# Kernel tuning notes

Measured on AMD Instinct MI355X. Metric: run time of the kernel, lower is better.

The kernel has to match this reference:

```python
import jax, jax.numpy as jnp
import numpy as np

D_MODEL = 1024
N_HEADS = 16
HEAD_DIM = D_MODEL // N_HEADS


def setup_inputs() -> dict:
    key = jax.random.key(0)
    k_x, k_q, k_k, k_v = jax.random.split(key, 4)
    B, S = 2, 2048
    x = jax.random.normal(k_x, (B, S, D_MODEL), dtype=jnp.float32)
    # nn.Linear weights stored as [out, in]; we apply x @ W.T
    scale = 1.0 / np.sqrt(D_MODEL)
    W_q = jax.random.uniform(k_q, (D_MODEL, D_MODEL), jnp.float32, -scale, scale)
    W_k = jax.random.uniform(k_k, (D_MODEL, D_MODEL), jnp.float32, -scale, scale)
    W_v = jax.random.uniform(k_v, (D_MODEL, D_MODEL), jnp.float32, -scale, scale)
    return {"x": x, "W_q": W_q, "W_k": W_k, "W_v": W_v}


def reference(x, W_q, W_k, W_v):
    B, S, D = x.shape
    H, Hd = N_HEADS, HEAD_DIM
    # QKV projections (Linear with no bias): x @ W.T
    Q = (x @ W_q.T).reshape(B, S, H, Hd).transpose(0, 2, 1, 3)  # [B,H,S,Hd]
    K = (x @ W_k.T).reshape(B, S, H, Hd).transpose(0, 2, 1, 3)
    V = (x @ W_v.T).reshape(B, S, H, Hd).transpose(0, 2, 1, 3)
    scores = jnp.einsum("bhqd,bhkd->bhqk", Q, K) / jnp.sqrt(jnp.float32(Hd))
    attn = jax.nn.softmax(scores, axis=-1)
    out = jnp.einsum("bhqk,bhkd->bhqd", attn, V)  # [B,H,S,Hd]
    return out.transpose(0, 2, 1, 3).reshape(B, S, H * Hd)
```

## Files before the change

kernel.cpp:

```cpp
#include <hip/hip_runtime.h>
#include <stdint.h>


typedef __bf16 bf16x8 __attribute__((ext_vector_type(8)));
typedef __bf16 bf16x4 __attribute__((ext_vector_type(4)));
typedef float  f32x4  __attribute__((ext_vector_type(4)));

#define D_MODEL 1024
#define SEQ     2048
#define NHEAD   16
#define HDIM    64
#define BS      4096

__device__ __forceinline__ void load_lds16(const void* g, void* lds) {
  __builtin_amdgcn_global_load_lds(
      (__attribute__((address_space(1))) void*)(uintptr_t)g,
      (__attribute__((address_space(3))) void*)(uintptr_t)lds,
      16, 0, 0);
}

__global__ void cvt_f32_bf16(const float* __restrict__ in,
                             __bf16* __restrict__ out, int n4) {
  int i = blockIdx.x * blockDim.x + threadIdx.x;
  if (i < n4) {
    float4 v = ((const float4*)in)[i];
    bf16x4 o;
    o[0] = (__bf16)v.x; o[1] = (__bf16)v.y;
    o[2] = (__bf16)v.z; o[3] = (__bf16)v.w;
    ((bf16x4*)out)[i] = o;
  }
}

__global__ __launch_bounds__(256) void qkv_gemm(
    const __bf16* __restrict__ X,
    const __bf16* __restrict__ Wq, const __bf16* __restrict__ Wk,
    const __bf16* __restrict__ Wv,
    __bf16* __restrict__ Qb, __bf16* __restrict__ Kb, __bf16* __restrict__ Vt) {
  __shared__ __bf16 As[128 * 32];
  __shared__ __bf16 Bs[128 * 32];

  const __bf16* W = (blockIdx.z == 0) ? Wq : (blockIdx.z == 1) ? Wk : Wv;

  const int t    = threadIdx.x;
  const int wv   = t >> 6;
  const int lane = t & 63;
  const int l15  = lane & 15;
  const int quad = lane >> 4;
  const int m0   = blockIdx.y * 128;
  const int n0   = blockIdx.x * 128;
  const int wm   = (wv >> 1) * 64;
  const int wn   = (wv & 1) * 64;

  f32x4 acc[4][4] = {};

  for (int it = 0; it < 32; ++it) {
    const int k0 = it * 32;
#pragma unroll
    for (int p = 0; p < 2; ++p) {
      const int c   = p * 256 + t;
      const int row = c >> 2;
      const int ko  = (c & 3) * 8;
      const unsigned lb = (unsigned)((p * 256 + wv * 64) * 16);
      load_lds16(X + (size_t)(m0 + row) * D_MODEL + k0 + ko, (char*)As + lb);
      load_lds16(W + (size_t)(n0 + row) * D_MODEL + k0 + ko, (char*)Bs + lb);
    }
    __syncthreads();

    bf16x8 af[4], bfb[4];
#pragma unroll
    for (int i = 0; i < 4; ++i)
      af[i] = *(const bf16x8*)&As[(wm + i * 16 + l15) * 32 + quad * 8];
#pragma unroll
    for (int j = 0; j < 4; ++j)
      bfb[j] = *(const bf16x8*)&Bs[(wn + j * 16 + l15) * 32 + quad * 8];
#pragma unroll
    for (int i = 0; i < 4; ++i)
#pragma unroll
      for (int j = 0; j < 4; ++j)
        acc[i][j] = __builtin_amdgcn_mfma_f32_16x16x32_bf16(af[i], bfb[j],
                                                            acc[i][j], 0, 0, 0);
    __syncthreads();
  }

  if (blockIdx.z != 2) {
    __bf16* Out = (blockIdx.z == 0) ? Qb : Kb;
#pragma unroll
    for (int i = 0; i < 4; ++i) {
      const int rg = m0 + wm + i * 16 + quad * 4;
#pragma unroll
      for (int j = 0; j < 4; ++j) {
        const int cg = n0 + wn + j * 16 + l15;
#pragma unroll
        for (int r = 0; r < 4; ++r)
          Out[(size_t)(rg + r) * D_MODEL + cg] = (__bf16)acc[i][j][r];
      }
    }
  } else {
#pragma unroll
    for (int i = 0; i < 4; ++i) {
      const int mg = m0 + wm + i * 16 + quad * 4;
#pragma unroll
      for (int j = 0; j < 4; ++j) {
        const int ng = n0 + wn + j * 16 + l15;
        bf16x4 v;
#pragma unroll
        for (int r = 0; r < 4; ++r) v[r] = (__bf16)acc[i][j][r];
        *(bf16x4*)&Vt[(size_t)ng * BS + mg] = v;
      }
    }
  }
}

__global__ __launch_bounds__(256) void attn(
    const __bf16* __restrict__ Qb, const __bf16* __restrict__ Kb,
    const __bf16* __restrict__ Vt, float* __restrict__ out) {
  __shared__ __bf16 Ks[64 * 64];
  __shared__ __bf16 Vs[64 * 64];
  __shared__ __bf16 Ps[4][16][72];

  const int t    = threadIdx.x;
  const int wv   = t >> 6;
  const int lane = t & 63;
  const int l15  = lane & 15;
  const int quad = lane >> 4;
  const int h    = blockIdx.y;
  const size_t bo = (size_t)blockIdx.z * SEQ;
  const int q0   = blockIdx.x * 64 + wv * 16;
  const int hd0  = h * HDIM;

  bf16x8 qf[2];
#pragma unroll
  for (int c = 0; c < 2; ++c) {
    qf[c] = *(const bf16x8*)&Qb[(bo + q0 + l15) * D_MODEL + hd0 + c * 32 + quad * 8];
#pragma unroll
    for (int j = 0; j < 8; ++j)
      qf[c][j] = (__bf16)(0.125f * (float)qf[c][j]);
  }

  float lsum[4] = {0.f, 0.f, 0.f, 0.f};
  f32x4 o_acc[4] = {};

  const int swz = quad ^ (l15 & 7);
  const int swz4 = (quad + 4) ^ (l15 & 7);

  for (int kt = 0; kt < SEQ / 64; ++kt) {
    const int n0 = kt * 64;
#pragma unroll
    for (int p = 0; p < 2; ++p) {
      const int c   = p * 256 + t;
      const int row = c >> 3;
      const int cc  = (c & 7) ^ (row & 7);
      const unsigned lb = (unsigned)((p * 256 + wv * 64) * 16);
      load_lds16(Kb + (bo + n0 + row) * D_MODEL + hd0 + cc * 8, (char*)Ks + lb);
      load_lds16(Vt + (size_t)(hd0 + row) * BS + bo + n0 + cc * 8, (char*)Vs + lb);
    }
    __syncthreads();

    f32x4 s[4] = {};
#pragma unroll
    for (int nt = 0; nt < 4; ++nt) {
      const int r = nt * 16 + l15;
      bf16x8 kf0 = *(const bf16x8*)&Ks[(r * 8 + swz) * 8];
      bf16x8 kf1 = *(const bf16x8*)&Ks[(r * 8 + swz4) * 8];
      s[nt] = __builtin_amdgcn_mfma_f32_16x16x32_bf16(qf[0], kf0, s[nt], 0, 0, 0);
      s[nt] = __builtin_amdgcn_mfma_f32_16x16x32_bf16(qf[1], kf1, s[nt], 0, 0, 0);
    }

#pragma unroll
    for (int nt = 0; nt < 4; ++nt)
#pragma unroll
      for (int r = 0; r < 4; ++r) {
        float p = __expf(s[nt][r]);
        lsum[r] += p;
        Ps[wv][quad * 4 + r][nt * 16 + l15] = (__bf16)p;
      }

    bf16x8 pf0 = *(const bf16x8*)&Ps[wv][l15][quad * 8];
    bf16x8 pf1 = *(const bf16x8*)&Ps[wv][l15][32 + quad * 8];

#pragma unroll
    for (int tt = 0; tt < 4; ++tt) {
      const int r = tt * 16 + l15;
      bf16x8 vf0 = *(const bf16x8*)&Vs[(r * 8 + swz) * 8];
      bf16x8 vf1 = *(const bf16x8*)&Vs[(r * 8 + swz4) * 8];
      o_acc[tt] = __builtin_amdgcn_mfma_f32_16x16x32_bf16(pf0, vf0, o_acc[tt], 0, 0, 0);
      o_acc[tt] = __builtin_amdgcn_mfma_f32_16x16x32_bf16(pf1, vf1, o_acc[tt], 0, 0, 0);
    }
    __syncthreads();
  }

#pragma unroll
  for (int r = 0; r < 4; ++r) {
    float s = lsum[r];
    s += __shfl_xor(s, 1);
    s += __shfl_xor(s, 2);
    s += __shfl_xor(s, 4);
    s += __shfl_xor(s, 8);
    lsum[r] = s;
  }

#pragma unroll
  for (int r = 0; r < 4; ++r) {
    float inv = 1.f / lsum[r];
    const size_t row = bo + q0 + quad * 4 + r;
#pragma unroll
    for (int tt = 0; tt < 4; ++tt)
      out[row * D_MODEL + hd0 + tt * 16 + l15] = o_acc[tt][r] * inv;
  }
}

extern "C" void kernel_launch(void* const* d_in, const int* in_sizes, int n_in,
                              void* d_out, int out_size, void* d_ws, size_t ws_size,
                              hipStream_t stream) {
  const float* x  = (const float*)d_in[0];
  const float* Wq = (const float*)d_in[1];
  const float* Wk = (const float*)d_in[2];
  const float* Wv = (const float*)d_in[3];
  float* out = (float*)d_out;

  char* ws = (char*)d_ws;
  __bf16* xb  = (__bf16*)(ws);
  __bf16* wqb = (__bf16*)(ws + (8u  << 20));
  __bf16* wkb = (__bf16*)(ws + (10u << 20));
  __bf16* wvb = (__bf16*)(ws + (12u << 20));
  __bf16* Qbf = (__bf16*)(ws + (14u << 20));
  __bf16* Kbf = (__bf16*)(ws + (22u << 20));
  __bf16* Vt  = (__bf16*)(ws + (30u << 20));

  cvt_f32_bf16<<<4096, 256, 0, stream>>>(x,  xb,  4194304 / 4);
  cvt_f32_bf16<<<1024, 256, 0, stream>>>(Wq, wqb, 1048576 / 4);
  cvt_f32_bf16<<<1024, 256, 0, stream>>>(Wk, wkb, 1048576 / 4);
  cvt_f32_bf16<<<1024, 256, 0, stream>>>(Wv, wvb, 1048576 / 4);

  qkv_gemm<<<dim3(8, 32, 3), 256, 0, stream>>>(xb, wqb, wkb, wvb, Qbf, Kbf, Vt);

  attn<<<dim3(SEQ / 64, NHEAD, 2), 256, 0, stream>>>(Qbf, Kbf, Vt, out);
}
```

Before: 175.1 us.

## Double query rows per attention wave, fuse conversion kernels, fold Q scale into GEMM

The attention kernel now gives each wave 32 query rows instead of 16. Each K/V tile loaded into LDS is reused across twice as many queries, and the block count is halved. The four f32-to-bf16 conversion launches are merged into one kernel, and the 1/sqrt(d) scale moves into the Q projection epilogue instead of being applied per block in attention. Register pressure rises and the grid shrinks to 512 blocks, which may lower occupancy.

```diff
diff --git a/kernel.cpp b/kernel.cpp
--- a/kernel.cpp
+++ b/kernel.cpp
@@ -19,16 +19,23 @@
       16, 0, 0);
 }
 
-__global__ void cvt_f32_bf16(const float* __restrict__ in,
-                             __bf16* __restrict__ out, int n4) {
+#define NX4 1048576
+#define NW4 262144
+__global__ void cvt_all(const float* __restrict__ x,  const float* __restrict__ wq,
+                        const float* __restrict__ wk, const float* __restrict__ wv,
+                        __bf16* __restrict__ xb,  __bf16* __restrict__ wqb,
+                        __bf16* __restrict__ wkb, __bf16* __restrict__ wvb) {
   int i = blockIdx.x * blockDim.x + threadIdx.x;
-  if (i < n4) {
-    float4 v = ((const float4*)in)[i];
-    bf16x4 o;
-    o[0] = (__bf16)v.x; o[1] = (__bf16)v.y;
-    o[2] = (__bf16)v.z; o[3] = (__bf16)v.w;
-    ((bf16x4*)out)[i] = o;
-  }
+  const float* in; __bf16* out; int j;
+  if (i < NX4)                { in = x;  out = xb;  j = i; }
+  else if (i < NX4 + NW4)     { in = wq; out = wqb; j = i - NX4; }
+  else if (i < NX4 + 2*NW4)   { in = wk; out = wkb; j = i - NX4 - NW4; }
+  else                        { in = wv; out = wvb; j = i - NX4 - 2*NW4; }
+  float4 v = ((const float4*)in)[j];
+  bf16x4 o;
+  o[0] = (__bf16)v.x; o[1] = (__bf16)v.y;
+  o[2] = (__bf16)v.z; o[3] = (__bf16)v.w;
+  ((bf16x4*)out)[j] = o;
 }
 
 __global__ __launch_bounds__(256) void qkv_gemm(
@@ -84,6 +91,7 @@
 
   if (blockIdx.z != 2) {
     __bf16* Out = (blockIdx.z == 0) ? Qb : Kb;
+    const float qs = (blockIdx.z == 0) ? 0.125f : 1.0f;
 #pragma unroll
     for (int i = 0; i < 4; ++i) {
       const int rg = m0 + wm + i * 16 + quad * 4;
@@ -92,7 +100,7 @@
         const int cg = n0 + wn + j * 16 + l15;
 #pragma unroll
         for (int r = 0; r < 4; ++r)
-          Out[(size_t)(rg + r) * D_MODEL + cg] = (__bf16)acc[i][j][r];
+          Out[(size_t)(rg + r) * D_MODEL + cg] = (__bf16)(acc[i][j][r] * qs);
       }
     }
   } else {
@@ -116,7 +124,7 @@
     const __bf16* __restrict__ Vt, float* __restrict__ out) {
   __shared__ __bf16 Ks[64 * 64];
   __shared__ __bf16 Vs[64 * 64];
-  __shared__ __bf16 Ps[4][16][72];
+  __shared__ __bf16 Ps[4][32][72];
 
   const int t    = threadIdx.x;
   const int wv   = t >> 6;
@@ -125,22 +133,21 @@
   const int quad = lane >> 4;
   const int h    = blockIdx.y;
   const size_t bo = (size_t)blockIdx.z * SEQ;
-  const int q0   = blockIdx.x * 64 + wv * 16;
+  const int q0   = blockIdx.x * 128 + wv * 32;
   const int hd0  = h * HDIM;
 
-  bf16x8 qf[2];
-#pragma unroll
-  for (int c = 0; c < 2; ++c) {
-    qf[c] = *(const bf16x8*)&Qb[(bo + q0 + l15) * D_MODEL + hd0 + c * 32 + quad * 8];
-#pragma unroll
-    for (int j = 0; j < 8; ++j)
-      qf[c][j] = (__bf16)(0.125f * (float)qf[c][j]);
-  }
-
-  float lsum[4] = {0.f, 0.f, 0.f, 0.f};
-  f32x4 o_acc[4] = {};
-
-  const int swz = quad ^ (l15 & 7);
+  bf16x8 qf[2][2];
+#pragma unroll
+  for (int hh = 0; hh < 2; ++hh)
+#pragma unroll
+    for (int c = 0; c < 2; ++c)
+      qf[hh][c] = *(const bf16x8*)&Qb[(bo + q0 + hh * 16 + l15) * D_MODEL +
+                                      hd0 + c * 32 + quad * 8];
+
+  float lsum[2][4] = {};
+  f32x4 o_acc[2][4] = {};
+
+  const int swz  = quad ^ (l15 & 7);
   const int swz4 = (quad + 4) ^ (l15 & 7);
 
   for (int kt = 0; kt < SEQ / 64; ++kt) {
@@ -156,57 +163,61 @@
     }
     __syncthreads();
 
-    f32x4 s[4] = {};
+    f32x4 s[2][4] = {};
 #pragma unroll
     for (int nt = 0; nt < 4; ++nt) {
       const int r = nt * 16 + l15;
       bf16x8 kf0 = *(const bf16x8*)&Ks[(r * 8 + swz) * 8];
       bf16x8 kf1 = *(const bf16x8*)&Ks[(r * 8 + swz4) * 8];
-      s[nt] = __builtin_amdgcn_mfma_f32_16x16x32_bf16(qf[0], kf0, s[nt], 0, 0, 0);
-      s[nt] = __builtin_amdgcn_mfma_f32_16x16x32_bf16(qf[1], kf1, s[nt], 0, 0, 0);
-    }
-
-#pragma unroll
-    for (int nt = 0; nt < 4; ++nt)
-#pragma unroll
-      for (int r = 0; r < 4; ++r) {
-        float p = __expf(s[nt][r]);
-        lsum[r] += p;
-        Ps[wv][quad * 4 + r][nt * 16 + l15] = (__bf16)p;
-      }
-
-    bf16x8 pf0 = *(const bf16x8*)&Ps[wv][l15][quad * 8];
-    bf16x8 pf1 = *(const bf16x8*)&Ps[wv][l15][32 + quad * 8];
+#pragma unroll
+      for (int hh = 0; hh < 2; ++hh) {
+        s[hh][nt] = __builtin_amdgcn_mfma_f32_16x16x32_bf16(qf[hh][0], kf0, s[hh][nt], 0, 0, 0);
+        s[hh][nt] = __builtin_amdgcn_mfma_f32_16x16x32_bf16(qf[hh][1], kf1, s[hh][nt], 0, 0, 0);
+      }
+    }
+
+#pragma unroll
+    for (int hh = 0; hh < 2; ++hh)
+#pragma unroll
+      for (int nt = 0; nt < 4; ++nt)
+#pragma unroll
+        for (int r = 0; r < 4; ++r) {
+          float p = __expf(s[hh][nt][r]);
+          lsum[hh][r] += p;
+          Ps[wv][hh * 16 + quad * 4 + r][nt * 16 + l15] = (__bf16)p;
+        }
 
 #pragma unroll
     for (int tt = 0; tt < 4; ++tt) {
       const int r = tt * 16 + l15;
       bf16x8 vf0 = *(const bf16x8*)&Vs[(r * 8 + swz) * 8];
       bf16x8 vf1 = *(const bf16x8*)&Vs[(r * 8 + swz4) * 8];
-      o_acc[tt] = __builtin_amdgcn_mfma_f32_16x16x32_bf16(pf0, vf0, o_acc[tt], 0, 0, 0);
-      o_acc[tt] = __builtin_amdgcn_mfma_f32_16x16x32_bf16(pf1, vf1, o_acc[tt], 0, 0, 0);
+#pragma unroll
+      for (int hh = 0; hh < 2; ++hh) {
+        bf16x8 pf0 = *(const bf16x8*)&Ps[wv][hh * 16 + l15][quad * 8];
+        bf16x8 pf1 = *(const bf16x8*)&Ps[wv][hh * 16 + l15][32 + quad * 8];
+        o_acc[hh][tt] = __builtin_amdgcn_mfma_f32_16x16x32_bf16(pf0, vf0, o_acc[hh][tt], 0, 0, 0);
+        o_acc[hh][tt] = __builtin_amdgcn_mfma_f32_16x16x32_bf16(pf1, vf1, o_acc[hh][tt], 0, 0, 0);
+      }
     }
     __syncthreads();
   }
 
 #pragma unroll
-  for (int r = 0; r < 4; ++r) {
-    float s = lsum[r];
-    s += __shfl_xor(s, 1);
-    s += __shfl_xor(s, 2);
-    s += __shfl_xor(s, 4);
-    s += __shfl_xor(s, 8);
-    lsum[r] = s;
-  }
-
-#pragma unroll
-  for (int r = 0; r < 4; ++r) {
-    float inv = 1.f / lsum[r];
-    const size_t row = bo + q0 + quad * 4 + r;
-#pragma unroll
-    for (int tt = 0; tt < 4; ++tt)
-      out[row * D_MODEL + hd0 + tt * 16 + l15] = o_acc[tt][r] * inv;
-  }
+  for (int hh = 0; hh < 2; ++hh)
+#pragma unroll
+    for (int r = 0; r < 4; ++r) {
+      float s = lsum[hh][r];
+      s += __shfl_xor(s, 1);
+      s += __shfl_xor(s, 2);
+      s += __shfl_xor(s, 4);
+      s += __shfl_xor(s, 8);
+      float inv = 1.f / s;
+      const size_t row = bo + q0 + hh * 16 + quad * 4 + r;
+#pragma unroll
+      for (int tt = 0; tt < 4; ++tt)
+        out[row * D_MODEL + hd0 + tt * 16 + l15] = o_acc[hh][tt][r] * inv;
+    }
 }
 
 extern "C" void kernel_launch(void* const* d_in, const int* in_sizes, int n_in,
@@ -227,12 +238,10 @@
   __bf16* Kbf = (__bf16*)(ws + (22u << 20));
   __bf16* Vt  = (__bf16*)(ws + (30u << 20));
 
-  cvt_f32_bf16<<<4096, 256, 0, stream>>>(x,  xb,  4194304 / 4);
-  cvt_f32_bf16<<<1024, 256, 0, stream>>>(Wq, wqb, 1048576 / 4);
-  cvt_f32_bf16<<<1024, 256, 0, stream>>>(Wk, wkb, 1048576 / 4);
-  cvt_f32_bf16<<<1024, 256, 0, stream>>>(Wv, wvb, 1048576 / 4);
+  cvt_all<<<(NX4 + 3 * NW4) / 256, 256, 0, stream>>>(x, Wq, Wk, Wv,
+                                                     xb, wqb, wkb, wvb);
 
   qkv_gemm<<<dim3(8, 32, 3), 256, 0, stream>>>(xb, wqb, wkb, wvb, Qbf, Kbf, Vt);
 
-  attn<<<dim3(SEQ / 64, NHEAD, 2), 256, 0, stream>>>(Qbf, Kbf, Vt, out);
-}
+  attn<<<dim3(SEQ / 128, NHEAD, 2), 256, 0, stream>>>(Qbf, Kbf, Vt, out);
+}
```

New measurement: 171.9 us. No clear change (-1.8%).
